# Optimization experiments

Measured on AMD Instinct MI355X. Metric: run time of the kernel, lower is better.

## Reference

```python
import jax, jax.numpy as jnp
import numpy as np

B, S, D = 16, 2048, 1024
E2 = 2 * 2048  # embed_dim * 2 FFN hidden
EPS = 1e-5


def layernorm(x, g, b):
    mu = jnp.mean(x, axis=-1, keepdims=True)
    var = jnp.mean(jnp.square(x - mu), axis=-1, keepdims=True)
    return (x - mu) * jax.lax.rsqrt(var + EPS) * g + b


def setup_inputs() -> dict:
    key = jax.random.key(0)
    ks = jax.random.split(key, 4)
    lags = jax.random.normal(ks[0], (B, S, D), dtype=jnp.float32)
    W1 = jax.random.normal(ks[1], (D, E2), dtype=jnp.float32) * (1.0 / np.sqrt(D))
    b1 = jnp.zeros((E2,), dtype=jnp.float32)
    W2 = jax.random.normal(ks[2], (E2, D), dtype=jnp.float32) * (1.0 / np.sqrt(E2))
    b2 = jnp.zeros((D,), dtype=jnp.float32)
    g1 = jnp.ones((D,), dtype=jnp.float32)
    be1 = jnp.zeros((D,), dtype=jnp.float32)
    g3 = jnp.ones((D,), dtype=jnp.float32)
    be3 = jnp.zeros((D,), dtype=jnp.float32)
    return {"lags": lags, "W1": W1, "b1": b1, "W2": W2, "b2": b2,
            "g1": g1, "be1": be1, "g3": g3, "be3": be3}


def reference(lags, W1, b1, W2, b2, g1, be1, g3, be3):
    # manual self-attention: scores = lags @ lags^T / sqrt(D)  -> [B,S,S]
    scale = 1.0 / jnp.sqrt(jnp.asarray(D, dtype=lags.dtype))
    scores = jnp.einsum('bsd,btd->bst', lags, lags) * scale
    attn = jax.nn.softmax(scores, axis=-1)
    attn_out = jnp.einsum('bst,btd->bsd', attn, lags)  # [B,S,D]
    x = layernorm(lags + attn_out, g1, be1)
    # FFN: Linear -> exact GELU -> Linear (dropout=0)
    h = jax.nn.gelu(jnp.einsum('bsd,de->bse', x, W1) + b1, approximate=False)
    ff = jnp.einsum('bse,ed->bsd', h, W2) + b2
    return layernorm(x + ff, g3, be3)
```

## Files before the change

kernel.cpp:

```cpp
#include <hip/hip_runtime.h>
#include <hip/hip_bf16.h>
#include <cmath>


typedef __bf16 bf16;
typedef __attribute__((ext_vector_type(8))) __bf16 bf16x8;
typedef __attribute__((ext_vector_type(4))) __bf16 bf16x4;
typedef __attribute__((ext_vector_type(4))) float f32x4;

static constexpr int kB  = 16;
static constexpr int kS  = 2048;
static constexpr int kD  = 1024;
static constexpr int kE2 = 4096;
static constexpr int kCB = 8;
static constexpr int kFR = 16384;

__device__ __forceinline__ void gload_lds16(const bf16* g, bf16* l) {
    __builtin_amdgcn_global_load_lds(
        (const __attribute__((address_space(1))) void*)g,
        (__attribute__((address_space(3))) void*)l,
        16, 0, 0);
}

__global__ __launch_bounds__(256) void cvt_bf16_kernel(const float* __restrict__ in,
                                                       bf16* __restrict__ out) {
    size_t i = ((size_t)blockIdx.x * 256 + threadIdx.x) * 4;
    float4 v = *(const float4*)(in + i);
    bf16x4 o;
    o.x = (bf16)v.x; o.y = (bf16)v.y; o.z = (bf16)v.z; o.w = (bf16)v.w;
    *(bf16x4*)(out + i) = o;
}

__global__ void transpose_cvt_kernel(const float* __restrict__ in, bf16* __restrict__ out,
                                     int R, int C, long long sIn, long long sOut) {
    __shared__ float tile[32][33];
    in  += (size_t)blockIdx.z * sIn;
    out += (size_t)blockIdx.z * sOut;
    const int c0 = blockIdx.x * 32, r0 = blockIdx.y * 32;
    const int tx = threadIdx.x, ty = threadIdx.y;
#pragma unroll
    for (int k = 0; k < 32; k += 8)
        tile[ty + k][tx] = in[(size_t)(r0 + ty + k) * C + (c0 + tx)];
    __syncthreads();
#pragma unroll
    for (int k = 0; k < 32; k += 8)
        out[(size_t)(c0 + ty + k) * R + (r0 + tx)] = (bf16)tile[tx][ty + k];
}

template <int MODE>
__global__ __launch_bounds__(512, 2)
void gemm_bt_kernel(const bf16* __restrict__ A, const bf16* __restrict__ Bm,
                    float* __restrict__ C, bf16* __restrict__ Cb,
                    const float* __restrict__ bias,
                    const float* __restrict__ resF, const bf16* __restrict__ resB,
                    int N, int K,
                    long long sA, long long sB, long long sC, long long sRes,
                    float scale) {
    __shared__ __align__(16) bf16 lds[2][2][2][256 * 32];
    const int tid  = threadIdx.x;
    const int lane = tid & 63;
    const int wv   = tid >> 6;
    const int wm   = wv >> 2;
    const int wn   = wv & 3;
    const int quad = lane >> 4, l15 = lane & 15;
    const int quadS = quad ^ ((l15 >> 1) & 3);
    const long long z = blockIdx.z;
    const bf16* Ab = A  + z * sA + (size_t)blockIdx.y * 256 * K;
    const bf16* Bb = Bm + z * sB + (size_t)blockIdx.x * 256 * K;

    const int srow = wv * 32 + (lane >> 2);
    const int scol = ((lane & 3) ^ ((lane >> 3) & 3)) * 8;
    const bf16* gA = Ab + (size_t)srow * K + scol;
    const bf16* gB = Bb + (size_t)srow * K + scol;
    const int NT = K >> 6;

    f32x4 acc[8][4];
#pragma unroll
    for (int i = 0; i < 8; i++)
#pragma unroll
        for (int j = 0; j < 4; j++) {
            f32x4 zv = {0.0f, 0.0f, 0.0f, 0.0f};
            acc[i][j] = zv;
        }

#define STAGE_HALF(h_)                                                        \
    do {                                                                      \
        const int t_ = (h_) >> 2, sel_ = (h_) & 3;                            \
        const bf16* g_ = ((sel_ & 1) ? gB : gA) + t_ * 64 + (sel_ >> 1) * 32; \
        bf16* l_ = &lds[t_ & 1][sel_ & 1][sel_ >> 1][wv * 32 * 32];           \
        gload_lds16(g_, l_);                                                  \
        gload_lds16(g_ + (size_t)16 * K, l_ + 16 * 32);                       \
    } while (0)

#define GPHASE(BUF, KS, QM, READB, VM)                                        \
    do {                                                                      \
        if (READB) {                                                          \
            _Pragma("unroll")                                                 \
            for (int nf = 0; nf < 4; nf++)                                    \
                bfr[nf] = *(const bf16x8*)&lds[BUF][1][KS][                   \
                    (wn * 64 + nf * 16 + l15) * 32 + quadS * 8];              \
        }                                                                     \
        _Pragma("unroll")                                                     \
        for (int mf = 0; mf < 4; mf++)                                        \
            afr[mf] = *(const bf16x8*)&lds[BUF][0][KS][                       \
                (wm * 128 + (QM * 4 + mf) * 16 + l15) * 32 + quadS * 8];      \
        if (h < 4 * NT) STAGE_HALF(h);                                        \
        h++;                                                                  \
        asm volatile("" ::: "memory");                                        \
        __builtin_amdgcn_s_barrier();                                         \
        asm volatile("s_waitcnt lgkmcnt(0)" ::: "memory");                    \
        __builtin_amdgcn_sched_barrier(0);                                    \
        __builtin_amdgcn_s_setprio(1);                                        \
        _Pragma("unroll")                                                     \
        for (int mf = 0; mf < 4; mf++)                                        \
            _Pragma("unroll")                                                 \
            for (int nf = 0; nf < 4; nf++)                                    \
                acc[QM * 4 + mf][nf] = __builtin_amdgcn_mfma_f32_16x16x32_bf16( \
                    afr[mf], bfr[nf], acc[QM * 4 + mf][nf], 0, 0, 0);         \
        __builtin_amdgcn_s_setprio(0);                                        \
        if (VM) asm volatile("s_waitcnt vmcnt(6)" ::: "memory");              \
        __builtin_amdgcn_s_barrier();                                         \
        asm volatile("" ::: "memory");                                        \
    } while (0)

    bf16x8 afr[4], bfr[4];
    int h = 0;
#pragma unroll
    for (int p = 0; p < 6; p++) { STAGE_HALF(h); h++; }
    asm volatile("s_waitcnt vmcnt(4)" ::: "memory");
    __builtin_amdgcn_s_barrier();
    asm volatile("" ::: "memory");

    for (int i = 0; i < NT / 2; i++) {
        GPHASE(0, 0, 0, true,  false);
        GPHASE(0, 0, 1, false, true);
        GPHASE(0, 1, 0, true,  false);
        GPHASE(0, 1, 1, false, true);
        GPHASE(1, 0, 0, true,  false);
        GPHASE(1, 0, 1, false, true);
        GPHASE(1, 1, 0, true,  false);
        GPHASE(1, 1, 1, false, true);
    }
#undef GPHASE
#undef STAGE_HALF

    const size_t m0 = (size_t)blockIdx.y * 256 + wm * 128;
    const size_t n0 = (size_t)blockIdx.x * 256 + wn * 64;
#pragma unroll
    for (int nf = 0; nf < 4; nf++) {
        const size_t col = n0 + nf * 16 + l15;
        const float bcol = (MODE == 2 || MODE == 3) ? bias[col] : 0.0f;
#pragma unroll
        for (int mf = 0; mf < 8; mf++) {
#pragma unroll
            for (int rr = 0; rr < 4; rr++) {
                const size_t row = m0 + mf * 16 + quad * 4 + rr;
                const float v = acc[mf][nf][rr];
                if (MODE == 0) {
                    Cb[z * sC + row * N + col] = (bf16)(v * scale);
                } else if (MODE == 1) {
                    C[z * sC + row * N + col] = v + resF[z * sRes + row * N + col];
                } else if (MODE == 2) {
                    const float t = v + bcol;
                    const float gl = 0.5f * t * (1.0f + erff(t * 0.70710678118654752f));
                    Cb[row * N + col] = (bf16)gl;
                } else {
                    C[row * N + col] = v + bcol + (float)resB[row * N + col];
                }
            }
        }
    }
}

__global__ __launch_bounds__(256)
void softmax_bf16_kernel(bf16* __restrict__ SP) {
    __shared__ float red[8];
    const size_t row = blockIdx.x;
    bf16* p = SP + row * kS;
    const int tid = threadIdx.x;
    bf16x8 v = *(const bf16x8*)(p + tid * 8);
    float f[8];
#pragma unroll
    for (int i = 0; i < 8; i++) f[i] = (float)v[i];
    float m = f[0];
#pragma unroll
    for (int i = 1; i < 8; i++) m = fmaxf(m, f[i]);
#pragma unroll
    for (int o = 32; o > 0; o >>= 1) m = fmaxf(m, __shfl_down(m, o, 64));
    if ((tid & 63) == 0) red[tid >> 6] = m;
    __syncthreads();
    m = fmaxf(fmaxf(red[0], red[1]), fmaxf(red[2], red[3]));
    float e[8], s = 0.0f;
#pragma unroll
    for (int i = 0; i < 8; i++) { e[i] = __expf(f[i] - m); s += e[i]; }
#pragma unroll
    for (int o = 32; o > 0; o >>= 1) s += __shfl_down(s, o, 64);
    __syncthreads();
    if ((tid & 63) == 0) red[4 + (tid >> 6)] = s;
    __syncthreads();
    s = red[4] + red[5] + red[6] + red[7];
    const float inv = 1.0f / s;
    bf16x8 o;
#pragma unroll
    for (int i = 0; i < 8; i++) o[i] = (bf16)(e[i] * inv);
    *(bf16x8*)(p + tid * 8) = o;
}

__global__ __launch_bounds__(256)
void layernorm_kernel(const float* __restrict__ in, const float* __restrict__ g,
                      const float* __restrict__ be, float* __restrict__ outF,
                      bf16* __restrict__ outB) {
    __shared__ float red[8];
    const size_t row = blockIdx.x;
    const float* src = in + row * kD;
    const int tid = threadIdx.x;
    float4 v = *(const float4*)(src + tid * 4);
    float s = v.x + v.y + v.z + v.w;
#pragma unroll
    for (int o = 32; o > 0; o >>= 1) s += __shfl_down(s, o, 64);
    if ((tid & 63) == 0) red[tid >> 6] = s;
    __syncthreads();
    const float mu = (red[0] + red[1] + red[2] + red[3]) * (1.0f / kD);
    const float d0 = v.x - mu, d1 = v.y - mu, d2 = v.z - mu, d3 = v.w - mu;
    float ss = d0 * d0 + d1 * d1 + d2 * d2 + d3 * d3;
#pragma unroll
    for (int o = 32; o > 0; o >>= 1) ss += __shfl_down(ss, o, 64);
    __syncthreads();
    if ((tid & 63) == 0) red[4 + (tid >> 6)] = ss;
    __syncthreads();
    const float var = (red[4] + red[5] + red[6] + red[7]) * (1.0f / kD);
    const float rstd = rsqrtf(var + 1e-5f);
    float4 gg = *(const float4*)(g + tid * 4);
    float4 bb = *(const float4*)(be + tid * 4);
    float4 o;
    o.x = d0 * rstd * gg.x + bb.x;
    o.y = d1 * rstd * gg.y + bb.y;
    o.z = d2 * rstd * gg.z + bb.z;
    o.w = d3 * rstd * gg.w + bb.w;
    if (outF) *(float4*)(outF + row * kD + tid * 4) = o;
    if (outB) {
        bf16x4 ob;
        ob.x = (bf16)o.x; ob.y = (bf16)o.y; ob.z = (bf16)o.z; ob.w = (bf16)o.w;
        *(bf16x4*)(outB + row * kD + tid * 4) = ob;
    }
}

extern "C" void kernel_launch(void* const* d_in, const int* in_sizes, int n_in,
                              void* d_out, int out_size, void* d_ws, size_t ws_size,
                              hipStream_t stream) {
    const float* lags = (const float*)d_in[0];
    const float* W1   = (const float*)d_in[1];
    const float* b1   = (const float*)d_in[2];
    const float* W2   = (const float*)d_in[3];
    const float* b2   = (const float*)d_in[4];
    const float* g1   = (const float*)d_in[5];
    const float* be1  = (const float*)d_in[6];
    const float* g3   = (const float*)d_in[7];
    const float* be3  = (const float*)d_in[8];
    float* out = (float*)d_out;

    const size_t REQUIRED = (size_t)(64 + 8 + 8 + 64 + 64) * 1024 * 1024;
    if (ws_size < REQUIRED) return;

    char* w = (char*)d_ws;
    bf16* lagsb = (bf16*)w; w += (size_t)kB * kS * kD * 2;
    bf16* W1T   = (bf16*)w; w += (size_t)kD * kE2 * 2;
    bf16* W2T   = (bf16*)w; w += (size_t)kE2 * kD * 2;
    bf16* lagsT = (bf16*)w; w += (size_t)kB * kD * kS * 2;
    bf16* SP    = (bf16*)w;
    bf16* xb    = lagsb;
    bf16* h     = lagsT;

    const int n = kB * kS * kD;

    cvt_bf16_kernel<<<n / 1024, 256, 0, stream>>>(lags, lagsb);
    transpose_cvt_kernel<<<dim3(kD / 32, kS / 32, kB), dim3(32, 8), 0, stream>>>(
        lags, lagsT, kS, kD, (long long)kS * kD, (long long)kD * kS);
    transpose_cvt_kernel<<<dim3(kE2 / 32, kD / 32, 1), dim3(32, 8), 0, stream>>>(
        W1, W1T, kD, kE2, 0, 0);
    transpose_cvt_kernel<<<dim3(kD / 32, kE2 / 32, 1), dim3(32, 8), 0, stream>>>(
        W2, W2T, kE2, kD, 0, 0);

    for (int c = 0; c < kB / kCB; c++) {
        const size_t off = (size_t)c * kCB * kS * kD;
        gemm_bt_kernel<0><<<dim3(kS / 256, kS / 256, kCB), 512, 0, stream>>>(
            lagsb + off, lagsb + off, nullptr, SP, nullptr, nullptr, nullptr,
            kS, kD, (long long)kS * kD, (long long)kS * kD, (long long)kS * kS, 0, 0.03125f);
        softmax_bf16_kernel<<<kCB * kS, 256, 0, stream>>>(SP);
        gemm_bt_kernel<1><<<dim3(kD / 256, kS / 256, kCB), 512, 0, stream>>>(
            SP, lagsT + off, out + off, nullptr, nullptr, lags + off, nullptr,
            kD, kS, (long long)kS * kS, (long long)kD * kS,
            (long long)kS * kD, (long long)kS * kD, 1.0f);
        layernorm_kernel<<<kCB * kS, 256, 0, stream>>>(out + off, g1, be1, nullptr, xb + off);
    }

    for (int c = 0; c < (kB * kS) / kFR; c++) {
        const size_t roff = (size_t)c * kFR * kD;
        gemm_bt_kernel<2><<<dim3(kE2 / 256, kFR / 256, 1), 512, 0, stream>>>(
            xb + roff, W1T, nullptr, h, b1, nullptr, nullptr,
            kE2, kD, 0, 0, 0, 0, 1.0f);
        gemm_bt_kernel<3><<<dim3(kD / 256, kFR / 256, 1), 512, 0, stream>>>(
            h, W2T, out + roff, nullptr, b2, nullptr, xb + roff,
            kD, kE2, 0, 0, 0, 0, 1.0f);
    }

    layernorm_kernel<<<kB * kS, 256, 0, stream>>>(out, g3, be3, out, nullptr);
}
```

Measured before the change: 1.524 ms.

## Remap GEMM blocks across XCDs and statically unroll the LDS prefetch pipeline

Block indices are remapped so that consecutive linear blocks are spread in groups of eight, which targets better L2 locality across the XCD chiplets. The staging logic no longer uses a runtime counter and a per-phase guard. Staging addresses are computed from precomputed LDS pointers, with an explicit prologue, steady-state loop and epilogue, and vmcnt waits placed where needed. This reduces scalar and address overhead in the main loop, at the cost of more complex, less flexible code that assumes the block count is a multiple of eight.

```diff
diff --git a/kernel.cpp b/kernel.cpp
--- a/kernel.cpp
+++ b/kernel.cpp
@@ -57,6 +57,7 @@
                     long long sA, long long sB, long long sC, long long sRes,
                     float scale) {
     __shared__ __align__(16) bf16 lds[2][2][2][256 * 32];
+    bf16* Lb = &lds[0][0][0][0];
     const int tid  = threadIdx.x;
     const int lane = tid & 63;
     const int wv   = tid >> 6;
@@ -64,15 +65,29 @@
     const int wn   = wv & 3;
     const int quad = lane >> 4, l15 = lane & 15;
     const int quadS = quad ^ ((l15 >> 1) & 3);
-    const long long z = blockIdx.z;
-    const bf16* Ab = A  + z * sA + (size_t)blockIdx.y * 256 * K;
-    const bf16* Bb = Bm + z * sB + (size_t)blockIdx.x * 256 * K;
+
+    const unsigned gx = gridDim.x, gy = gridDim.y;
+    unsigned lin = blockIdx.x + gx * (blockIdx.y + gy * blockIdx.z);
+    const unsigned nper = (gx * gy * gridDim.z) >> 3;
+    lin = (lin & 7) * nper + (lin >> 3);
+    const unsigned bx = lin % gx;
+    const unsigned tq = lin / gx;
+    const unsigned by = tq % gy;
+    const long long z = tq / gy;
+
+    const bf16* Ab = A  + z * sA + (size_t)by * 256 * K;
+    const bf16* Bb = Bm + z * sB + (size_t)bx * 256 * K;
 
     const int srow = wv * 32 + (lane >> 2);
     const int scol = ((lane & 3) ^ ((lane >> 3) & 3)) * 8;
     const bf16* gA = Ab + (size_t)srow * K + scol;
     const bf16* gB = Bb + (size_t)srow * K + scol;
-    const int NT = K >> 6;
+    const size_t kk16 = (size_t)16 * K;
+    const int NTH = K >> 7;
+
+    const bf16* aP = Lb + ((wm * 128 + l15) * 32 + quadS * 8);
+    const bf16* bP = Lb + 16384 + ((wn * 64 + l15) * 32 + quadS * 8);
+    bf16* ldsW = Lb + wv * 1024;
 
     f32x4 acc[8][4];
 #pragma unroll
@@ -83,29 +98,28 @@
             acc[i][j] = zv;
         }
 
-#define STAGE_HALF(h_)                                                        \
+#define STG(GT, SEL, BUF)                                                     \
     do {                                                                      \
-        const int t_ = (h_) >> 2, sel_ = (h_) & 3;                            \
-        const bf16* g_ = ((sel_ & 1) ? gB : gA) + t_ * 64 + (sel_ >> 1) * 32; \
-        bf16* l_ = &lds[t_ & 1][sel_ & 1][sel_ >> 1][wv * 32 * 32];           \
+        const bf16* g_ = (((SEL) & 1) ? (GT##B) : (GT##A)) + ((SEL) >> 1) * 32; \
+        bf16* l_ = ldsW + (BUF) * 32768 + ((SEL) & 1) * 16384 + ((SEL) >> 1) * 8192; \
         gload_lds16(g_, l_);                                                  \
-        gload_lds16(g_ + (size_t)16 * K, l_ + 16 * 32);                       \
+        gload_lds16(g_ + kk16, l_ + 512);                                     \
     } while (0)
 
-#define GPHASE(BUF, KS, QM, READB, VM)                                        \
+#define VMC4 asm volatile("s_waitcnt vmcnt(4)" ::: "memory")
+#define VMC0 asm volatile("s_waitcnt vmcnt(0)" ::: "memory")
+
+#define GPHASE(BUF, KS, QM, READB, STG_STMT, WAIT_STMT)                       \
     do {                                                                      \
         if (READB) {                                                          \
             _Pragma("unroll")                                                 \
             for (int nf = 0; nf < 4; nf++)                                    \
-                bfr[nf] = *(const bf16x8*)&lds[BUF][1][KS][                   \
-                    (wn * 64 + nf * 16 + l15) * 32 + quadS * 8];              \
+                bfr[nf] = *(const bf16x8*)(bP + (BUF) * 32768 + (KS) * 8192 + nf * 512); \
         }                                                                     \
         _Pragma("unroll")                                                     \
         for (int mf = 0; mf < 4; mf++)                                        \
-            afr[mf] = *(const bf16x8*)&lds[BUF][0][KS][                       \
-                (wm * 128 + (QM * 4 + mf) * 16 + l15) * 32 + quadS * 8];      \
-        if (h < 4 * NT) STAGE_HALF(h);                                        \
-        h++;                                                                  \
+            afr[mf] = *(const bf16x8*)(aP + (BUF) * 32768 + (KS) * 8192 + ((QM) * 4 + mf) * 512); \
+        STG_STMT;                                                             \
         asm volatile("" ::: "memory");                                        \
         __builtin_amdgcn_s_barrier();                                         \
         asm volatile("s_waitcnt lgkmcnt(0)" ::: "memory");                    \
@@ -115,37 +129,59 @@
         for (int mf = 0; mf < 4; mf++)                                        \
             _Pragma("unroll")                                                 \
             for (int nf = 0; nf < 4; nf++)                                    \
-                acc[QM * 4 + mf][nf] = __builtin_amdgcn_mfma_f32_16x16x32_bf16( \
-                    afr[mf], bfr[nf], acc[QM * 4 + mf][nf], 0, 0, 0);         \
+                acc[(QM) * 4 + mf][nf] = __builtin_amdgcn_mfma_f32_16x16x32_bf16( \
+                    afr[mf], bfr[nf], acc[(QM) * 4 + mf][nf], 0, 0, 0);       \
         __builtin_amdgcn_s_setprio(0);                                        \
-        if (VM) asm volatile("s_waitcnt vmcnt(6)" ::: "memory");              \
-        __builtin_amdgcn_s_barrier();                                         \
+        WAIT_STMT;                                                            \
+        __builtin_amdgcn_s_barrier();                                        \
         asm volatile("" ::: "memory");                                        \
     } while (0)
 
     bf16x8 afr[4], bfr[4];
-    int h = 0;
-#pragma unroll
-    for (int p = 0; p < 6; p++) { STAGE_HALF(h); h++; }
-    asm volatile("s_waitcnt vmcnt(4)" ::: "memory");
-    __builtin_amdgcn_s_barrier();
-    asm volatile("" ::: "memory");
-
-    for (int i = 0; i < NT / 2; i++) {
-        GPHASE(0, 0, 0, true,  false);
-        GPHASE(0, 0, 1, false, true);
-        GPHASE(0, 1, 0, true,  false);
-        GPHASE(0, 1, 1, false, true);
-        GPHASE(1, 0, 0, true,  false);
-        GPHASE(1, 0, 1, false, true);
-        GPHASE(1, 1, 0, true,  false);
-        GPHASE(1, 1, 1, false, true);
+    {
+        const bf16* t0A = gA;      const bf16* t0B = gB;
+        const bf16* t1A = gA + 64; const bf16* t1B = gB + 64;
+        STG(t0, 0, 0); STG(t0, 1, 0); STG(t0, 2, 0); STG(t0, 3, 0);
+        STG(t1, 0, 1); STG(t1, 1, 1);
+        VMC4;
+        __builtin_amdgcn_s_barrier();
+        asm volatile("" ::: "memory");
+    }
+
+    for (int i = 0; i < NTH - 1; i++) {
+        const bf16* t1A = gA + (size_t)(2 * i + 1) * 64;
+        const bf16* t1B = gB + (size_t)(2 * i + 1) * 64;
+        const bf16* t2A = t1A + 64;  const bf16* t2B = t1B + 64;
+        const bf16* t3A = t1A + 128; const bf16* t3B = t1B + 128;
+        GPHASE(0, 0, 0, true,  STG(t1, 2, 1), (void)0);
+        GPHASE(0, 0, 1, false, STG(t1, 3, 1), (void)0);
+        GPHASE(0, 1, 0, true,  STG(t2, 0, 0), (void)0);
+        GPHASE(0, 1, 1, false, STG(t2, 1, 0), VMC4);
+        GPHASE(1, 0, 0, true,  STG(t2, 2, 0), (void)0);
+        GPHASE(1, 0, 1, false, STG(t2, 3, 0), (void)0);
+        GPHASE(1, 1, 0, true,  STG(t3, 0, 1), (void)0);
+        GPHASE(1, 1, 1, false, STG(t3, 1, 1), VMC4);
+    }
+    {
+        const int i = NTH - 1;
+        const bf16* t1A = gA + (size_t)(2 * i + 1) * 64;
+        const bf16* t1B = gB + (size_t)(2 * i + 1) * 64;
+        GPHASE(0, 0, 0, true,  STG(t1, 2, 1), (void)0);
+        GPHASE(0, 0, 1, false, STG(t1, 3, 1), (void)0);
+        GPHASE(0, 1, 0, true,  (void)0, (void)0);
+        GPHASE(0, 1, 1, false, (void)0, VMC0);
+        GPHASE(1, 0, 0, true,  (void)0, (void)0);
+        GPHASE(1, 0, 1, false, (void)0, (void)0);
+        GPHASE(1, 1, 0, true,  (void)0, (void)0);
+        GPHASE(1, 1, 1, false, (void)0, (void)0);
     }
 #undef GPHASE
-#undef STAGE_HALF
-
-    const size_t m0 = (size_t)blockIdx.y * 256 + wm * 128;
-    const size_t n0 = (size_t)blockIdx.x * 256 + wn * 64;
+#undef STG
+#undef VMC4
+#undef VMC0
+
+    const size_t m0 = (size_t)by * 256 + wm * 128;
+    const size_t n0 = (size_t)bx * 256 + wn * 64;
 #pragma unroll
     for (int nf = 0; nf < 4; nf++) {
         const size_t col = n0 + nf * 16 + l15;
```

After: 1.417 ms. 1.08x faster.
